# Performance work log

Hardware: AMD Instinct MI355X
Metric: run time of the kernel (lower is better)

The kernel has to match this reference:

```python
import jax, jax.numpy as jnp
import numpy as np
import math

V = 32000      # vocab_size
D = 1024       # hidden_dims
T_MAX = 1024   # max_txt_len
L = 4          # n_layers
H = 8          # heads (fixed in CausalMHA)
HD = D // H
B, T = 2, 1024
EPS = 1e-5


def setup_inputs() -> dict:
    key = jax.random.key(0)
    ks = jax.random.split(key, 20)
    s = 0.02
    inp = {
        "x": jax.random.randint(ks[0], (B, T), 0, V, dtype=jnp.int64) if jax.config.read("jax_enable_x64") else jax.random.randint(ks[0], (B, T), 0, V, dtype=jnp.int32),
        "tok_emb": jax.random.normal(ks[1], (V, D), jnp.float32) * s,
        "pos_emb": jax.random.normal(ks[2], (1, T_MAX, D), jnp.float32) * s,
        "ln1_g": jnp.ones((L, D), jnp.float32),
        "ln1_b": jnp.zeros((L, D), jnp.float32),
        "wqkv": jax.random.normal(ks[3], (L, D, 3 * D), jnp.float32) * s,
        "bqkv": jnp.zeros((L, 3 * D), jnp.float32),
        "wo": jax.random.normal(ks[4], (L, D, D), jnp.float32) * s,
        "bo": jnp.zeros((L, D), jnp.float32),
        "ln2_g": jnp.ones((L, D), jnp.float32),
        "ln2_b": jnp.zeros((L, D), jnp.float32),
        "wfc": jax.random.normal(ks[5], (L, D, 4 * D), jnp.float32) * s,   # no bias
        "wfc2": jax.random.normal(ks[6], (L, 4 * D, D), jnp.float32) * s,  # no bias
        "fn_g": jnp.ones((D,), jnp.float32),
        "fn_b": jnp.zeros((D,), jnp.float32),
        "wout": jax.random.normal(ks[7], (D, V), jnp.float32) * s,
        "bout": jnp.zeros((V,), jnp.float32),
    }
    return inp


def _ln(x, g, b):
    mu = jnp.mean(x, axis=-1, keepdims=True)
    var = jnp.var(x, axis=-1, keepdims=True)
    return (x - mu) * jax.lax.rsqrt(var + EPS) * g + b


def _attn(xn, wqkv_l, bqkv_l, wo_l, bo_l):
    Bb, Tt, _ = xn.shape
    qkv = xn @ wqkv_l + bqkv_l                      # [B,T,3D]
    q, k, v = jnp.split(qkv, 3, axis=-1)
    q = q.reshape(Bb, Tt, H, HD)
    k = k.reshape(Bb, Tt, H, HD)
    v = v.reshape(Bb, Tt, H, HD)
    scores = jnp.einsum("bqhd,bkhd->bhqk", q, k) / math.sqrt(HD)
    mask = jnp.triu(jnp.ones((Tt, Tt), bool), k=1)   # True above diagonal
    scores = jnp.where(mask, jnp.float32(-jnp.inf), scores)
    att = jax.nn.softmax(scores, axis=-1)
    out = jnp.einsum("bhqk,bkhd->bqhd", att, v).reshape(Bb, Tt, D)
    return out @ wo_l + bo_l


def reference(x, tok_emb, pos_emb, ln1_g, ln1_b, wqkv, bqkv, wo, bo,
              ln2_g, ln2_b, wfc, wfc2, fn_g, fn_b, wout, bout):
    Tt = x.shape[1]
    h = tok_emb[x] + pos_emb[:, :Tt, :]              # [B,T,D]
    for i in range(L):
        h = h + _attn(_ln(h, ln1_g[i], ln1_b[i]), wqkv[i], bqkv[i], wo[i], bo[i])
        hn = _ln(h, ln2_g[i], ln2_b[i])
        h = h + jax.nn.gelu(hn @ wfc[i], approximate=False) @ wfc2[i]
    h = _ln(h, fn_g, fn_b)
    return h @ wout + bout                           # [B,T,V] logits
```

## Files before the change

### kernel.cpp

```cpp
#include <hip/hip_runtime.h>
#include <math.h>
#include <stdint.h>

#define D_  1024
#define T_  1024
#define H_  8
#define HD_ 128
#define L_  4
#define V_  32000
#define M_  2048

typedef __attribute__((ext_vector_type(4))) float f32x4;
typedef __attribute__((ext_vector_type(4))) short s16x4;
typedef __attribute__((ext_vector_type(8))) short s16x8;
typedef unsigned short u16;

__device__ __forceinline__ u16 f2bf(float f) {
  union { float f; uint32_t u; } c; c.f = f;
  uint32_t r = c.u + 0x7fffu + ((c.u >> 16) & 1u);
  return (u16)(r >> 16);
}
__device__ __forceinline__ float bf2f(u16 h) {
  union { uint32_t u; float f; } c; c.u = ((uint32_t)h) << 16;
  return c.f;
}
__device__ __forceinline__ float gelu_f(float x) {
  return 0.5f * x * (1.0f + erff(x * 0.70710678118654752f));
}

__device__ __forceinline__ void gload16(const u16* g, u16* l) {
  __builtin_amdgcn_global_load_lds(
      (const __attribute__((address_space(1))) void*)(uintptr_t)g,
      (__attribute__((address_space(3))) void*)(uint32_t)(uintptr_t)l,
      16, 0, 0);
}

template<int INF32>
__global__ __launch_bounds__(256)
void convT_kernel(const void* __restrict__ inv, u16* __restrict__ out,
                  int ldin, int ldout, long inZ, long outZ)
{
  __shared__ __align__(16) u16 tile[64][72];
  const int c0 = blockIdx.x << 6, r0 = blockIdx.y << 6;
  const int t = threadIdx.x;
  const int rr = t >> 2, cs = (t & 3) << 4;
  u16 tmp[16];
  if (INF32) {
    const float* in = (const float*)inv + (size_t)blockIdx.z * inZ;
    const float* p = in + (size_t)(r0 + rr) * ldin + c0 + cs;
#pragma unroll
    for (int q = 0; q < 4; ++q) {
      f32x4 v = *(const f32x4*)(p + q * 4);
#pragma unroll
      for (int j = 0; j < 4; ++j) tmp[q * 4 + j] = f2bf(v[j]);
    }
  } else {
    const u16* in = (const u16*)inv + (size_t)blockIdx.z * inZ;
    const u16* p = in + (size_t)(r0 + rr) * ldin + c0 + cs;
    s16x8 v0 = *(const s16x8*)(p);
    s16x8 v1 = *(const s16x8*)(p + 8);
#pragma unroll
    for (int j = 0; j < 8; ++j) { tmp[j] = (u16)v0[j]; tmp[8 + j] = (u16)v1[j]; }
  }
  *(s16x8*)&tile[rr][cs]     = *(const s16x8*)tmp;
  *(s16x8*)&tile[rr][cs + 8] = *(const s16x8*)(tmp + 8);
  __syncthreads();
  const int cr = t >> 2, rs = (t & 3) << 4;
  u16 o[16];
#pragma unroll
  for (int j = 0; j < 16; ++j) o[j] = tile[rs + j][cr];
  u16* op = out + (size_t)blockIdx.z * outZ + (size_t)(c0 + cr) * ldout + r0 + rs;
  *(s16x8*)op       = *(const s16x8*)o;
  *(s16x8*)(op + 8) = *(const s16x8*)(o + 8);
}

template<int TM, int ACT, int BIAS, int OUT, int MODE>
__global__ __launch_bounds__(256)
void gemm2(const u16* __restrict__ A, const u16* __restrict__ Bw,
           const float* __restrict__ bias, const float* __restrict__ res,
           void* __restrict__ Cv,
           int K, int lda, int ldb, int ldc, float scale,
           long sAb, long sAh, long sBb, long sBh, long sCb, long sCh)
{
  static_assert(TM == 64 || TM == 128, "tile");
  constexpr int WN  = (TM == 128) ? 2 : 4;
  constexpr int WNW = 128 / WN;
  constexpr int NJ  = WNW / 16;
  constexpr int AR  = TM / 64;

  const int gx = gridDim.x, gy = gridDim.y;
  int flat = (blockIdx.z * gy + blockIdx.y) * gx + blockIdx.x;
  const int nwg = gx * gy * gridDim.z;
  int swz = (flat & 7) * (nwg >> 3) + (flat >> 3);
  const int bx = swz % gx; swz /= gx;
  const int by = swz % gy;
  const int z  = swz / gy;

  if (MODE == 1 && by > bx) return;
  const int m0 = bx * TM, n0 = by * 128;
  int ktiles = K >> 5;
  if (MODE == 2) { const int lim = (m0 + TM) >> 5; if (lim < ktiles) ktiles = lim; }

  const u16* Ab = A  + (size_t)(z >> 3) * sAb + (size_t)(z & 7) * sAh;
  const u16* Bb = Bw + (size_t)(z >> 3) * sBb + (size_t)(z & 7) * sBh;

  __shared__ __align__(16) u16 As[2][TM * 32];
  __shared__ __align__(16) u16 Bs[2][128 * 32];

  const int tid = threadIdx.x, lane = tid & 63, wave = tid >> 6;
  const int wm = wave / WN, wn = wave % WN;
  const int l15 = lane & 15, l4 = lane >> 4;
  const int srow = lane >> 2, scol = (lane & 3) << 3;

  f32x4 acc[4][NJ];
  const f32x4 z4 = {0.f, 0.f, 0.f, 0.f};
#pragma unroll
  for (int i = 0; i < 4; ++i)
#pragma unroll
    for (int j = 0; j < NJ; ++j) acc[i][j] = z4;

  auto stage = [&](int kt, int buf) {
    const int kc = (kt << 5) + scol;
#pragma unroll
    for (int r = 0; r < AR; ++r) {
      const int row = r * 64 + wave * 16;
      gload16(Ab + (size_t)(m0 + row + srow) * lda + kc, &As[buf][row * 32]);
    }
#pragma unroll
    for (int r = 0; r < 2; ++r) {
      const int row = r * 64 + wave * 16;
      gload16(Bb + (size_t)(n0 + row + srow) * ldb + kc, &Bs[buf][row * 32]);
    }
  };

  stage(0, 0);
  __syncthreads();

  for (int kt = 0; kt < ktiles; ++kt) {
    const int buf = kt & 1;
    if (kt + 1 < ktiles) stage(kt + 1, buf ^ 1);
    const u16* ap = &As[buf][(wm * 64 + l15) * 32 + (l4 << 3)];
    const u16* bp = &Bs[buf][(wn * WNW + l15) * 32 + (l4 << 3)];
    s16x8 af[4], bf[NJ];
#pragma unroll
    for (int i = 0; i < 4; ++i) af[i] = *(const s16x8*)(ap + i * (16 * 32));
#pragma unroll
    for (int j = 0; j < NJ; ++j) bf[j] = *(const s16x8*)(bp + j * (16 * 32));
#pragma unroll
    for (int i = 0; i < 4; ++i)
#pragma unroll
      for (int j = 0; j < NJ; ++j)
        acc[i][j] = __builtin_amdgcn_mfma_f32_16x16x32_bf16(af[i], bf[j], acc[i][j], 0, 0, 0);
    __syncthreads();
  }

  const size_t cbase = (size_t)(z >> 3) * sCb + (size_t)(z & 7) * sCh;
  float* Cf = (float*)Cv;
  u16*   Ch = (u16*)Cv;
#pragma unroll
  for (int i = 0; i < 4; ++i) {
    const int row0 = m0 + wm * 64 + i * 16 + l4 * 4;
#pragma unroll
    for (int j = 0; j < NJ; ++j) {
      const int col = n0 + wn * WNW + j * 16 + l15;
      const float bv = BIAS ? bias[col] : 0.0f;
#pragma unroll
      for (int r = 0; r < 4; ++r) {
        float v = acc[i][j][r] * scale + bv;
        if (ACT) v = gelu_f(v);
        const size_t idx = cbase + (size_t)(row0 + r) * ldc + col;
        if (OUT == 0)      Ch[idx] = f2bf(v);
        else if (OUT == 1) Cf[idx] = v;
        else               Cf[idx] = v + res[idx];
      }
    }
  }
}

__global__ __launch_bounds__(512, 2)
void gemm8_logits(const u16* __restrict__ A, const u16* __restrict__ Bw,
                  const float* __restrict__ bias, float* __restrict__ C)
{
  int flat = blockIdx.x;
  int swz = (flat & 7) * 125 + (flat >> 3);
  const int bx = swz & 7;
  const int by = swz >> 3;
  const int m0 = bx << 8, n0 = by << 8;

  __shared__ __align__(16) u16 lds[65536];

  const int tid = threadIdx.x, lane = tid & 63, wave = tid >> 6;
  const int wm = wave >> 2, wn = wave & 3;
  const int l15 = lane & 15, l4 = lane >> 4;

  f32x4 acc[8][4];
  const f32x4 z4 = {0.f, 0.f, 0.f, 0.f};
#pragma unroll
  for (int i = 0; i < 8; ++i)
#pragma unroll
    for (int j = 0; j < 4; ++j) acc[i][j] = z4;

  auto stg = [&](const u16* G, int rowbase, int slot, int kt, int kh) {
    if (kt >= 16) return;
#pragma unroll
    for (int r = 0; r < 2; ++r) {
      const int u = r * 512 + (wave << 6) + lane;
      const int rw = u >> 2, ks = u & 3;
      const int ksw = ks ^ ((rw >> 1) & 3);
      const u16* src = G + (size_t)(rowbase + rw) * 1024 + (kt << 6) + (kh << 5) + (ksw << 3);
      gload16(src, &lds[slot + r * 4096 + (wave << 9)]);
    }
  };

  s16x8 af[4], bfr[4];

#define LDA4(bb, kk, mh)                                                      \
  {                                                                           \
    _Pragma("unroll") for (int f = 0; f < 4; ++f) {                           \
      const int rw = wm * 128 + (mh) * 64 + f * 16 + l15;                     \
      af[f] = *(const s16x8*)&lds[(bb) + (kk) * 8192 + rw * 32 +              \
                                  ((l4 ^ ((rw >> 1) & 3)) << 3)];             \
    }                                                                         \
  }
#define LDB4(bb, kk)                                                          \
  {                                                                           \
    _Pragma("unroll") for (int f = 0; f < 4; ++f) {                           \
      const int rn = wn * 64 + f * 16 + l15;                                  \
      bfr[f] = *(const s16x8*)&lds[(bb) + 16384 + (kk) * 8192 + rn * 32 +     \
                                   ((l4 ^ ((rn >> 1) & 3)) << 3)];            \
    }                                                                         \
  }
#define MFMA16(mh)                                                            \
  {                                                                           \
    __builtin_amdgcn_s_barrier();                                             \
    asm volatile("s_waitcnt lgkmcnt(0)" ::: "memory");                        \
    __builtin_amdgcn_sched_barrier(0);                                        \
    __builtin_amdgcn_s_setprio(1);                                            \
    _Pragma("unroll") for (int f = 0; f < 4; ++f)                             \
      _Pragma("unroll") for (int nf = 0; nf < 4; ++nf)                        \
        acc[(mh) * 4 + f][nf] = __builtin_amdgcn_mfma_f32_16x16x32_bf16(      \
            af[f], bfr[nf], acc[(mh) * 4 + f][nf], 0, 0, 0);                  \
    __builtin_amdgcn_s_setprio(0);                                            \
  }
#define BAR() __builtin_amdgcn_s_barrier()
#define VM4() asm volatile("s_waitcnt vmcnt(4)" ::: "memory")

  stg(A,  m0, 0,             0, 0);
  stg(Bw, n0, 16384,         0, 0);
  stg(A,  m0, 8192,          0, 1);
  stg(Bw, n0, 16384 + 8192,  0, 1);
  stg(A,  m0, 32768,         1, 0);
  stg(Bw, n0, 32768 + 16384, 1, 0);
  VM4();
  BAR();

  for (int i = 0; i < 8; ++i) {
    const int t = 2 * i;
    LDA4(0, 0, 0); LDB4(0, 0);
    stg(A, m0, 32768 + 8192, t + 1, 1);
    MFMA16(0); BAR();
    LDA4(0, 0, 1);
    stg(Bw, n0, 32768 + 24576, t + 1, 1);
    MFMA16(1); BAR();
    LDA4(0, 1, 0); LDB4(0, 1);
    stg(A, m0, 0, t + 2, 0);
    MFMA16(0); BAR();
    LDA4(0, 1, 1);
    stg(Bw, n0, 16384, t + 2, 0);
    MFMA16(1); VM4(); BAR();
    LDA4(32768, 0, 0); LDB4(32768, 0);
    stg(A, m0, 8192, t + 2, 1);
    MFMA16(0); BAR();
    LDA4(32768, 0, 1);
    stg(Bw, n0, 16384 + 8192, t + 2, 1);
    MFMA16(1); BAR();
    LDA4(32768, 1, 0); LDB4(32768, 1);
    stg(A, m0, 32768, t + 3, 0);
    MFMA16(0); BAR();
    LDA4(32768, 1, 1);
    stg(Bw, n0, 32768 + 16384, t + 3, 0);
    MFMA16(1); VM4(); BAR();
  }
#undef LDA4
#undef LDB4
#undef MFMA16
#undef BAR
#undef VM4

  float bv[4];
#pragma unroll
  for (int nf = 0; nf < 4; ++nf) bv[nf] = bias[n0 + wn * 64 + nf * 16 + l15];
#pragma unroll
  for (int mf = 0; mf < 8; ++mf) {
    const int row0 = m0 + wm * 128 + mf * 16 + l4 * 4;
#pragma unroll
    for (int nf = 0; nf < 4; ++nf) {
      const int col = n0 + wn * 64 + nf * 16 + l15;
#pragma unroll
      for (int r = 0; r < 4; ++r)
        C[(size_t)(row0 + r) * V_ + col] = acc[mf][nf][r] + bv[nf];
    }
  }
}

__global__ __launch_bounds__(256)
void ln_bf16(const float* __restrict__ x, const float* __restrict__ g,
             const float* __restrict__ b, u16* __restrict__ y)
{
  __shared__ float red[8];
  const int row = blockIdx.x, tid = threadIdx.x;
  f32x4 v = *(const f32x4*)&x[(size_t)row * D_ + tid * 4];
  float s  = v[0] + v[1] + v[2] + v[3];
  float s2 = v[0]*v[0] + v[1]*v[1] + v[2]*v[2] + v[3]*v[3];
#pragma unroll
  for (int off = 32; off > 0; off >>= 1) {
    s  += __shfl_xor(s, off);
    s2 += __shfl_xor(s2, off);
  }
  if ((tid & 63) == 0) { red[tid >> 6] = s; red[4 + (tid >> 6)] = s2; }
  __syncthreads();
  s  = red[0] + red[1] + red[2] + red[3];
  s2 = red[4] + red[5] + red[6] + red[7];
  const float mean = s * (1.0f / D_);
  const float var  = s2 * (1.0f / D_) - mean * mean;
  const float rs   = rsqrtf(var + 1e-5f);
  f32x4 gg = *(const f32x4*)&g[tid * 4];
  f32x4 bb = *(const f32x4*)&b[tid * 4];
  u16 o[4];
#pragma unroll
  for (int j = 0; j < 4; ++j) o[j] = f2bf((v[j] - mean) * rs * gg[j] + bb[j]);
  *(s16x4*)&y[(size_t)row * D_ + tid * 4] = *(const s16x4*)o;
}

__global__ __launch_bounds__(256)
void softmax_bf16(u16* __restrict__ S)
{
  const int rI = blockIdx.x * 4 + (threadIdx.x >> 6);
  const int lane = threadIdx.x & 63;
  const int q = rI & (T_ - 1);
  u16* row = S + (size_t)rI * T_;
  s16x8 v0 = *(const s16x8*)&row[lane * 16];
  s16x8 v1 = *(const s16x8*)&row[lane * 16 + 8];
  float s[16];
  float mx = -1e30f;
#pragma unroll
  for (int j = 0; j < 16; ++j) {
    const int c = lane * 16 + j;
    const u16 raw = (u16)(j < 8 ? v0[j] : v1[j - 8]);
    s[j] = (c <= q) ? bf2f(raw) : -1e30f;
    mx = fmaxf(mx, s[j]);
  }
#pragma unroll
  for (int off = 32; off > 0; off >>= 1) mx = fmaxf(mx, __shfl_xor(mx, off));
  float sum = 0.f;
#pragma unroll
  for (int j = 0; j < 16; ++j) {
    s[j] = (lane * 16 + j <= q) ? __expf(s[j] - mx) : 0.f;
    sum += s[j];
  }
#pragma unroll
  for (int off = 32; off > 0; off >>= 1) sum += __shfl_xor(sum, off);
  const float inv = 1.0f / sum;
  s16x8 o0, o1;
#pragma unroll
  for (int j = 0; j < 8; ++j) {
    o0[j] = (short)f2bf(s[j] * inv);
    o1[j] = (short)f2bf(s[j + 8] * inv);
  }
  *(s16x8*)&row[lane * 16]     = o0;
  *(s16x8*)&row[lane * 16 + 8] = o1;
}

__global__ __launch_bounds__(256)
void embed_kernel(const int* __restrict__ x, const float* __restrict__ tok,
                  const float* __restrict__ pos, float* __restrict__ h)
{
  const int row = blockIdx.x, tid = threadIdx.x;
  const int t = row & (T_ - 1);
  const int id = x[row];
  f32x4 a = *(const f32x4*)&tok[(size_t)id * D_ + tid * 4];
  f32x4 p = *(const f32x4*)&pos[(size_t)t * D_ + tid * 4];
  f32x4 o = {a[0] + p[0], a[1] + p[1], a[2] + p[2], a[3] + p[3]};
  *(f32x4*)&h[(size_t)row * D_ + tid * 4] = o;
}

extern "C" void kernel_launch(void* const* d_in, const int* in_sizes, int n_in,
                              void* d_out, int out_size, void* d_ws, size_t ws_size,
                              hipStream_t stream)
{
  (void)in_sizes; (void)n_in; (void)out_size; (void)ws_size;
  const int*   x     = (const int*)  d_in[0];
  const float* tok   = (const float*)d_in[1];
  const float* pos   = (const float*)d_in[2];
  const float* ln1_g = (const float*)d_in[3];
  const float* ln1_b = (const float*)d_in[4];
  const float* wqkv  = (const float*)d_in[5];
  const float* bqkv  = (const float*)d_in[6];
  const float* wo    = (const float*)d_in[7];
  const float* bo    = (const float*)d_in[8];
  const float* ln2_g = (const float*)d_in[9];
  const float* ln2_b = (const float*)d_in[10];
  const float* wfc   = (const float*)d_in[11];
  const float* wfc2  = (const float*)d_in[12];
  const float* fn_g  = (const float*)d_in[13];
  const float* fn_b  = (const float*)d_in[14];
  const float* wout  = (const float*)d_in[15];
  const float* bout  = (const float*)d_in[16];
  float* out = (float*)d_out;

  float* h  = (float*)d_ws;
  u16* xn   = (u16*)(h + (size_t)M_ * D_);
  u16* Wq   = xn  + (size_t)M_ * D_;
  u16* Wo   = Wq  + (size_t)3 * D_ * D_;
  u16* Wf1  = Wo  + (size_t)D_ * D_;
  u16* Wf2  = Wf1 + (size_t)4 * D_ * D_;
  u16* qkv  = Wf2 + (size_t)4 * D_ * D_;
  u16* Vt   = qkv + (size_t)M_ * 3 * D_;
  u16* S    = Vt  + (size_t)2 * T_ * D_;
  u16* WoutT = Wq;

  const long sQb = (long)T_ * 3 * D_;
  const long sSb = (long)8 * T_ * T_;
  const long sSh = (long)T_ * T_;
  const float iscale = 0.08838834764831845f;

  embed_kernel<<<M_, 256, 0, stream>>>(x, tok, pos, h);

  for (int l = 0; l < L_; ++l) {
    convT_kernel<1><<<dim3(48, 16, 1), 256, 0, stream>>>(
        wqkv + (size_t)l * D_ * 3 * D_, Wq, 3 * D_, D_, 0, 0);
    convT_kernel<1><<<dim3(16, 16, 1), 256, 0, stream>>>(
        wo + (size_t)l * D_ * D_, Wo, D_, D_, 0, 0);
    convT_kernel<1><<<dim3(64, 16, 1), 256, 0, stream>>>(
        wfc + (size_t)l * D_ * 4 * D_, Wf1, 4 * D_, D_, 0, 0);
    convT_kernel<1><<<dim3(16, 64, 1), 256, 0, stream>>>(
        wfc2 + (size_t)l * 4 * D_ * D_, Wf2, D_, 4 * D_, 0, 0);

    ln_bf16<<<M_, 256, 0, stream>>>(h, ln1_g + l * D_, ln1_b + l * D_, xn);
    gemm2<128, 0, 1, 0, 0><<<dim3(16, 24, 1), 256, 0, stream>>>(
        xn, Wq, bqkv + l * 3 * D_, nullptr, qkv,
        D_, D_, D_, 3 * D_, 1.0f, 0, 0, 0, 0, 0, 0);
    gemm2<128, 0, 0, 0, 1><<<dim3(8, 8, 16), 256, 0, stream>>>(
        qkv, qkv + D_, nullptr, nullptr, S,
        HD_, 3 * D_, 3 * D_, T_, iscale,
        sQb, (long)HD_, sQb, (long)HD_, sSb, sSh);
    softmax_bf16<<<16 * T_ / 4, 256, 0, stream>>>(S);
    convT_kernel<0><<<dim3(16, 16, 2), 256, 0, stream>>>(
        qkv + 2 * D_, Vt, 3 * D_, T_, (long)T_ * 3 * D_, (long)T_ * D_);
    gemm2<64, 0, 0, 0, 2><<<dim3(16, 1, 16), 256, 0, stream>>>(
        S, Vt, nullptr, nullptr, xn,
        T_, T_, T_, D_, 1.0f,
        sSb, sSh, (long)T_ * D_, (long)HD_ * T_, (long)T_ * D_, (long)HD_);
    gemm2<64, 0, 1, 2, 0><<<dim3(32, 8, 1), 256, 0, stream>>>(
        xn, Wo, bo + l * D_, h, h,
        D_, D_, D_, D_, 1.0f, 0, 0, 0, 0, 0, 0);
    ln_bf16<<<M_, 256, 0, stream>>>(h, ln2_g + l * D_, ln2_b + l * D_, xn);
    gemm2<128, 1, 0, 0, 0><<<dim3(16, 32, 1), 256, 0, stream>>>(
        xn, Wf1, nullptr, nullptr, S,
        D_, D_, D_, 4 * D_, 1.0f, 0, 0, 0, 0, 0, 0);
    gemm2<64, 0, 0, 2, 0><<<dim3(32, 8, 1), 256, 0, stream>>>(
        S, Wf2, nullptr, h, h,
        4 * D_, 4 * D_, 4 * D_, D_, 1.0f, 0, 0, 0, 0, 0, 0);
  }

  ln_bf16<<<M_, 256, 0, stream>>>(h, fn_g, fn_b, xn);
  convT_kernel<1><<<dim3(500, 16, 1), 256, 0, stream>>>(
      wout, WoutT, V_, D_, 0, 0);
  gemm8_logits<<<1000, 512, 0, stream>>>(xn, WoutT, bout, out);
}
```

Baseline: 996.7 us.

## Replace separate QK^T, softmax and PV kernels with fused flash attention

```diff
diff --git a/kernel.cpp b/kernel.cpp
--- a/kernel.cpp
+++ b/kernel.cpp
@@ -74,13 +74,12 @@
   *(s16x8*)(op + 8) = *(const s16x8*)(o + 8);
 }
 
-template<int TM, int ACT, int BIAS, int OUT, int MODE>
+template<int TM, int ACT, int BIAS, int OUT>
 __global__ __launch_bounds__(256)
 void gemm2(const u16* __restrict__ A, const u16* __restrict__ Bw,
            const float* __restrict__ bias, const float* __restrict__ res,
            void* __restrict__ Cv,
-           int K, int lda, int ldb, int ldc, float scale,
-           long sAb, long sAh, long sBb, long sBh, long sCb, long sCh)
+           int K, int lda, int ldb, int ldc, float scale)
 {
   static_assert(TM == 64 || TM == 128, "tile");
   constexpr int WN  = (TM == 128) ? 2 : 4;
@@ -89,20 +88,14 @@
   constexpr int AR  = TM / 64;
 
   const int gx = gridDim.x, gy = gridDim.y;
-  int flat = (blockIdx.z * gy + blockIdx.y) * gx + blockIdx.x;
-  const int nwg = gx * gy * gridDim.z;
+  int flat = blockIdx.y * gx + blockIdx.x;
+  const int nwg = gx * gy;
   int swz = (flat & 7) * (nwg >> 3) + (flat >> 3);
-  const int bx = swz % gx; swz /= gx;
-  const int by = swz % gy;
-  const int z  = swz / gy;
-
-  if (MODE == 1 && by > bx) return;
+  const int bx = swz % gx;
+  const int by = swz / gx;
+
   const int m0 = bx * TM, n0 = by * 128;
-  int ktiles = K >> 5;
-  if (MODE == 2) { const int lim = (m0 + TM) >> 5; if (lim < ktiles) ktiles = lim; }
-
-  const u16* Ab = A  + (size_t)(z >> 3) * sAb + (size_t)(z & 7) * sAh;
-  const u16* Bb = Bw + (size_t)(z >> 3) * sBb + (size_t)(z & 7) * sBh;
+  const int ktiles = K >> 5;
 
   __shared__ __align__(16) u16 As[2][TM * 32];
   __shared__ __align__(16) u16 Bs[2][128 * 32];
@@ -124,12 +117,12 @@
 #pragma unroll
     for (int r = 0; r < AR; ++r) {
       const int row = r * 64 + wave * 16;
-      gload16(Ab + (size_t)(m0 + row + srow) * lda + kc, &As[buf][row * 32]);
+      gload16(A + (size_t)(m0 + row + srow) * lda + kc, &As[buf][row * 32]);
     }
 #pragma unroll
     for (int r = 0; r < 2; ++r) {
       const int row = r * 64 + wave * 16;
-      gload16(Bb + (size_t)(n0 + row + srow) * ldb + kc, &Bs[buf][row * 32]);
+      gload16(Bw + (size_t)(n0 + row + srow) * ldb + kc, &Bs[buf][row * 32]);
     }
   };
 
@@ -154,7 +147,6 @@
     __syncthreads();
   }
 
-  const size_t cbase = (size_t)(z >> 3) * sCb + (size_t)(z & 7) * sCh;
   float* Cf = (float*)Cv;
   u16*   Ch = (u16*)Cv;
 #pragma unroll
@@ -168,13 +160,157 @@
       for (int r = 0; r < 4; ++r) {
         float v = acc[i][j][r] * scale + bv;
         if (ACT) v = gelu_f(v);
-        const size_t idx = cbase + (size_t)(row0 + r) * ldc + col;
+        const size_t idx = (size_t)(row0 + r) * ldc + col;
         if (OUT == 0)      Ch[idx] = f2bf(v);
         else if (OUT == 1) Cf[idx] = v;
         else               Cf[idx] = v + res[idx];
       }
     }
   }
+}
+
+__global__ __launch_bounds__(256)
+void flash_attn(const u16* __restrict__ qkv, const u16* __restrict__ Vt,
+                u16* __restrict__ xo)
+{
+  const int qb = 15 - blockIdx.x;
+  const int z  = blockIdx.y;
+  const int b  = z >> 3, hh = z & 7;
+
+  __shared__ __align__(16) u16 Ks[64 * 128];
+  __shared__ __align__(16) u16 Vs[128 * 64];
+  __shared__ __align__(16) u16 Ps[64 * 80];
+
+  const int tid = threadIdx.x, lane = tid & 63, w = tid >> 6;
+  const int l15 = lane & 15, l4 = lane >> 4;
+  const float iscale = 0.08838834764831845f;
+
+  const int qrow = qb * 64 + w * 16 + l15;
+  const u16* qptr = qkv + ((size_t)(b * T_) + qrow) * (3 * D_) + hh * HD_;
+
+  s16x8 bQ[4];
+#pragma unroll
+  for (int ks = 0; ks < 4; ++ks)
+    bQ[ks] = *(const s16x8*)(qptr + ks * 32 + l4 * 8);
+
+  f32x4 O[8];
+#pragma unroll
+  for (int i = 0; i < 8; ++i) O[i] = {0.f, 0.f, 0.f, 0.f};
+  float m_run = -1e30f, l_run = 0.f;
+
+  const int ntiles = qb + 1;
+  for (int kt = 0; kt < ntiles; ++kt) {
+    __syncthreads();
+    {
+      const int r = tid >> 2, c = (tid & 3) << 5;
+      const u16* src = qkv + ((size_t)(b * T_) + kt * 64 + r) * (3 * D_) + D_ + hh * HD_ + c;
+#pragma unroll
+      for (int u = 0; u < 4; ++u) {
+        s16x8 v = *(const s16x8*)(src + u * 8);
+        const int dblk = (c >> 3) + u;
+        *(s16x8*)&Ks[r * 128 + ((dblk ^ (r & 7)) << 3)] = v;
+      }
+      const int d = tid >> 1, kc0 = (tid & 1) << 5;
+      const u16* vsrc = Vt + ((size_t)z * HD_ + d) * T_ + kt * 64 + kc0;
+#pragma unroll
+      for (int u = 0; u < 4; ++u) {
+        s16x8 v = *(const s16x8*)(vsrc + u * 8);
+        const int kblk = (kc0 >> 3) + u;
+        *(s16x8*)&Vs[d * 64 + ((kblk ^ (d & 7)) << 3)] = v;
+      }
+    }
+    __syncthreads();
+
+    f32x4 st[4];
+#pragma unroll
+    for (int mf = 0; mf < 4; ++mf) st[mf] = {0.f, 0.f, 0.f, 0.f};
+#pragma unroll
+    for (int ks = 0; ks < 4; ++ks) {
+      s16x8 aK[4];
+#pragma unroll
+      for (int mf = 0; mf < 4; ++mf) {
+        const int r = mf * 16 + l15;
+        aK[mf] = *(const s16x8*)&Ks[r * 128 + ((((ks << 2) + l4) ^ (r & 7)) << 3)];
+      }
+#pragma unroll
+      for (int mf = 0; mf < 4; ++mf)
+        st[mf] = __builtin_amdgcn_mfma_f32_16x16x32_bf16(aK[mf], bQ[ks], st[mf], 0, 0, 0);
+    }
+
+    const bool diag = (kt == qb);
+    float sv[16];
+    float mx = -1e30f;
+#pragma unroll
+    for (int mf = 0; mf < 4; ++mf)
+#pragma unroll
+      for (int r = 0; r < 4; ++r) {
+        float s = st[mf][r] * iscale;
+        if (diag) {
+          const int k = kt * 64 + mf * 16 + l4 * 4 + r;
+          if (k > qrow) s = -1e30f;
+        }
+        sv[mf * 4 + r] = s;
+        mx = fmaxf(mx, s);
+      }
+    mx = fmaxf(mx, __shfl_xor(mx, 16));
+    mx = fmaxf(mx, __shfl_xor(mx, 32));
+    const float m_new = fmaxf(m_run, mx);
+    const float sc_old = __expf(m_run - m_new);
+    float psum = 0.f;
+    u16 pb[16];
+#pragma unroll
+    for (int j = 0; j < 16; ++j) {
+      const float p = __expf(sv[j] - m_new);
+      psum += p;
+      pb[j] = f2bf(p);
+    }
+    psum += __shfl_xor(psum, 16);
+    psum += __shfl_xor(psum, 32);
+    l_run = l_run * sc_old + psum;
+    m_run = m_new;
+
+    float scr[4];
+#pragma unroll
+    for (int r = 0; r < 4; ++r) scr[r] = __shfl(sc_old, l4 * 4 + r);
+#pragma unroll
+    for (int df = 0; df < 8; ++df)
+#pragma unroll
+      for (int r = 0; r < 4; ++r) O[df][r] *= scr[r];
+
+    {
+      const int row = w * 16 + l15;
+#pragma unroll
+      for (int j = 0; j < 16; ++j) {
+        const int k = (j >> 2) * 16 + l4 * 4 + (j & 3);
+        Ps[row * 80 + (((k >> 3) ^ (l15 & 7)) << 3) + (k & 7)] = pb[j];
+      }
+    }
+
+#pragma unroll
+    for (int kc = 0; kc < 2; ++kc) {
+      const int prow = w * 16 + l15;
+      s16x8 aP = *(const s16x8*)&Ps[prow * 80 + ((((kc << 2) + l4) ^ (l15 & 7)) << 3)];
+#pragma unroll
+      for (int df = 0; df < 8; ++df) {
+        const int d = df * 16 + l15;
+        s16x8 bV = *(const s16x8*)&Vs[d * 64 + ((((kc << 2) + l4) ^ (d & 7)) << 3)];
+        O[df] = __builtin_amdgcn_mfma_f32_16x16x32_bf16(aP, bV, O[df], 0, 0, 0);
+      }
+    }
+  }
+
+  const float inv_l = 1.0f / l_run;
+  float invr[4];
+#pragma unroll
+  for (int r = 0; r < 4; ++r) invr[r] = __shfl(inv_l, l4 * 4 + r);
+#pragma unroll
+  for (int df = 0; df < 8; ++df)
+#pragma unroll
+    for (int r = 0; r < 4; ++r) {
+      const int row = qb * 64 + w * 16 + l4 * 4 + r;
+      xo[((size_t)(b * T_) + row) * D_ + hh * HD_ + df * 16 + l15] =
+          f2bf(O[df][r] * invr[r]);
+    }
 }
 
 __global__ __launch_bounds__(512, 2)
@@ -333,45 +469,6 @@
 }
 
 __global__ __launch_bounds__(256)
-void softmax_bf16(u16* __restrict__ S)
-{
-  const int rI = blockIdx.x * 4 + (threadIdx.x >> 6);
-  const int lane = threadIdx.x & 63;
-  const int q = rI & (T_ - 1);
-  u16* row = S + (size_t)rI * T_;
-  s16x8 v0 = *(const s16x8*)&row[lane * 16];
-  s16x8 v1 = *(const s16x8*)&row[lane * 16 + 8];
-  float s[16];
-  float mx = -1e30f;
-#pragma unroll
-  for (int j = 0; j < 16; ++j) {
-    const int c = lane * 16 + j;
-    const u16 raw = (u16)(j < 8 ? v0[j] : v1[j - 8]);
-    s[j] = (c <= q) ? bf2f(raw) : -1e30f;
-    mx = fmaxf(mx, s[j]);
-  }
-#pragma unroll
-  for (int off = 32; off > 0; off >>= 1) mx = fmaxf(mx, __shfl_xor(mx, off));
-  float sum = 0.f;
-#pragma unroll
-  for (int j = 0; j < 16; ++j) {
-    s[j] = (lane * 16 + j <= q) ? __expf(s[j] - mx) : 0.f;
-    sum += s[j];
-  }
-#pragma unroll
-  for (int off = 32; off > 0; off >>= 1) sum += __shfl_xor(sum, off);
-  const float inv = 1.0f / sum;
-  s16x8 o0, o1;
-#pragma unroll
-  for (int j = 0; j < 8; ++j) {
-    o0[j] = (short)f2bf(s[j] * inv);
-    o1[j] = (short)f2bf(s[j + 8] * inv);
-  }
-  *(s16x8*)&row[lane * 16]     = o0;
-  *(s16x8*)&row[lane * 16 + 8] = o1;
-}
-
-__global__ __launch_bounds__(256)
 void embed_kernel(const int* __restrict__ x, const float* __restrict__ tok,
                   const float* __restrict__ pos, float* __restrict__ h)
 {
@@ -419,11 +516,6 @@
   u16* S    = Vt  + (size_t)2 * T_ * D_;
   u16* WoutT = Wq;
 
-  const long sQb = (long)T_ * 3 * D_;
-  const long sSb = (long)8 * T_ * T_;
-  const long sSh = (long)T_ * T_;
-  const float iscale = 0.08838834764831845f;
-
   embed_kernel<<<M_, 256, 0, stream>>>(x, tok, pos, h);
 
   for (int l = 0; l < L_; ++l) {
@@ -437,30 +529,18 @@
         wfc2 + (size_t)l * 4 * D_ * D_, Wf2, D_, 4 * D_, 0, 0);
 
     ln_bf16<<<M_, 256, 0, stream>>>(h, ln1_g + l * D_, ln1_b + l * D_, xn);
-    gemm2<128, 0, 1, 0, 0><<<dim3(16, 24, 1), 256, 0, stream>>>(
-        xn, Wq, bqkv + l * 3 * D_, nullptr, qkv,
-        D_, D_, D_, 3 * D_, 1.0f, 0, 0, 0, 0, 0, 0);
-    gemm2<128, 0, 0, 0, 1><<<dim3(8, 8, 16), 256, 0, stream>>>(
-        qkv, qkv + D_, nullptr, nullptr, S,
-        HD_, 3 * D_, 3 * D_, T_, iscale,
-        sQb, (long)HD_, sQb, (long)HD_, sSb, sSh);
-    softmax_bf16<<<16 * T_ / 4, 256, 0, stream>>>(S);
+    gemm2<128, 0, 1, 0><<<dim3(16, 24), 256, 0, stream>>>(
+        xn, Wq, bqkv + l * 3 * D_, nullptr, qkv, D_, D_, D_, 3 * D_, 1.0f);
     convT_kernel<0><<<dim3(16, 16, 2), 256, 0, stream>>>(
         qkv + 2 * D_, Vt, 3 * D_, T_, (long)T_ * 3 * D_, (long)T_ * D_);
-    gemm2<64, 0, 0, 0, 2><<<dim3(16, 1, 16), 256, 0, stream>>>(
-        S, Vt, nullptr, nullptr, xn,
-        T_, T_, T_, D_, 1.0f,
-        sSb, sSh, (long)T_ * D_, (long)HD_ * T_, (long)T_ * D_, (long)HD_);
-    gemm2<64, 0, 1, 2, 0><<<dim3(32, 8, 1), 256, 0, stream>>>(
-        xn, Wo, bo + l * D_, h, h,
-        D_, D_, D_, D_, 1.0f, 0, 0, 0, 0, 0, 0);
+    flash_attn<<<dim3(16, 16), 256, 0, stream>>>(qkv, Vt, xn);
+    gemm2<64, 0, 1, 2><<<dim3(32, 8), 256, 0, stream>>>(
+        xn, Wo, bo + l * D_, h, h, D_, D_, D_, D_, 1.0f);
     ln_bf16<<<M_, 256, 0, stream>>>(h, ln2_g + l * D_, ln2_b + l * D_, xn);
-    gemm2<128, 1, 0, 0, 0><<<dim3(16, 32, 1), 256, 0, stream>>>(
-        xn, Wf1, nullptr, nullptr, S,
-        D_, D_, D_, 4 * D_, 1.0f, 0, 0, 0, 0, 0, 0);
-    gemm2<64, 0, 0, 2, 0><<<dim3(32, 8, 1), 256, 0, stream>>>(
-        S, Wf2, nullptr, h, h,
-        4 * D_, 4 * D_, 4 * D_, D_, 1.0f, 0, 0, 0, 0, 0, 0);
+    gemm2<128, 1, 0, 0><<<dim3(16, 32), 256, 0, stream>>>(
+        xn, Wf1, nullptr, nullptr, S, D_, D_, D_, 4 * D_, 1.0f);
+    gemm2<64, 0, 0, 2><<<dim3(32, 8), 256, 0, stream>>>(
+        S, Wf2, nullptr, h, h, 4 * D_, 4 * D_, 4 * D_, D_, 1.0f);
   }
 
   ln_bf16<<<M_, 256, 0, stream>>>(h, fn_g, fn_b, xn);
```

New measurement: 1.004 ms. About the same (+0.8%).
